# Kernel optimization log

Measured on AMD Instinct MI355X. Metric: run time of the kernel, lower is better.

The kernel has to match this reference:

```python
import jax, jax.numpy as jnp
import numpy as np

H, D_MODEL, D_K, D_V = 16, 1024, 64, 64
B, S = 4, 2048


def _xavier(key, shape):
    # xavier_uniform over last two dims (matches torch for 3D param: fan per matrix)
    fan_in, fan_out = shape[-2], shape[-1]
    limit = jnp.sqrt(6.0 / (fan_in + fan_out))
    return jax.random.uniform(key, shape, jnp.float32, -limit, limit)


def setup_inputs() -> dict:
    key = jax.random.key(0)
    kq, kk, kv, kwq, kwk, kwv, kwo = jax.random.split(key, 7)
    return {
        "Q": jax.random.normal(kq, (B, S, D_MODEL), jnp.float32),
        "K": jax.random.normal(kk, (B, S, D_MODEL), jnp.float32),
        "V": jax.random.normal(kv, (B, S, D_MODEL), jnp.float32),
        "W_Q": _xavier(kwq, (H, D_MODEL, D_K)),
        "W_K": _xavier(kwk, (H, D_MODEL, D_K)),
        "W_V": _xavier(kwv, (H, D_MODEL, D_V)),
        "W_O": _xavier(kwo, (H * D_V, D_MODEL)),
    }


def reference(Q, K, V, W_Q, W_K, W_V, W_O):
    # Per-head projections (batched over heads instead of Python loop)
    q = jnp.einsum("bsm,hmk->bhsk", Q, W_Q)  # [B,H,S,d_k]
    k = jnp.einsum("bsm,hmk->bhsk", K, W_K)  # [B,H,S,d_k]
    v = jnp.einsum("bsm,hmv->bhsv", V, W_V)  # [B,H,S,d_v]

    scale = 1.0 / jnp.sqrt(jnp.asarray(q.shape[-1], q.dtype))
    scores = jnp.einsum("bhqk,bhsk->bhqs", q, k) * scale  # [B,H,S,S]
    attn = jax.nn.softmax(scores, axis=-1)
    heads = jnp.einsum("bhqs,bhsv->bhqv", attn, v)  # [B,H,S,d_v]

    # concat heads along feature dim: [B,S,H*d_v]
    concat = jnp.transpose(heads, (0, 2, 1, 3)).reshape(Q.shape[0], Q.shape[1], -1)
    return concat @ W_O  # [B,S,d_model]
```

## Files before the change

### kernel.cpp

```cpp
#include <hip/hip_runtime.h>
#include <hip/hip_bf16.h>


typedef __attribute__((ext_vector_type(8))) short short8;
typedef __attribute__((ext_vector_type(4))) float floatx4;
typedef unsigned short u16;

#define NH 16
#define DM 1024
#define DK 64
#define NB 4
#define SS 2048

__device__ inline u16 f2bf(float f) {
    unsigned u = __builtin_bit_cast(unsigned, f);
    return (u16)((u + 0x7fffu + ((u >> 16) & 1u)) >> 16);
}

__device__ inline unsigned pk2(float a, float b) {
    unsigned r;
    asm("v_cvt_pk_bf16_f32 %0, %1, %2" : "=v"(r) : "v"(a), "v"(b));
    return r;
}

__device__ inline uint4 cvt8r(float4 lo, float4 hi) {
    uint4 r;
    r.x = pk2(lo.x, lo.y);
    r.y = pk2(lo.z, lo.w);
    r.z = pk2(hi.x, hi.y);
    r.w = pk2(hi.z, hi.w);
    return r;
}

__global__ __launch_bounds__(256) void prep_w(
    const float* __restrict__ W0, const float* __restrict__ W1,
    const float* __restrict__ W2, const float* __restrict__ WO,
    uint4* __restrict__ dst, int mode) {
    int idx = blockIdx.x * 256 + threadIdx.x;
    const int total = mode ? 128 * 1024 : 3 * 16 * 128 * 64;
    const int stride = gridDim.x * 256;
    for (; idx < total; idx += stride) {
        float v[8];
        if (mode == 0) {
            int n64 = idx & 63, kt = (idx >> 6) & 127;
            int h = (idx >> 13) & 15, w = idx >> 17;
            const float* src = (w == 0 ? W0 : (w == 1 ? W1 : W2)) +
                               ((size_t)(h * 1024 + kt * 8)) * 64 + n64;
#pragma unroll
            for (int j = 0; j < 8; j++) v[j] = src[(size_t)j * 64];
        } else {
            int n = idx & 1023, kt = idx >> 10;
            const float* src = WO + (size_t)(kt * 8) * 1024 + n;
#pragma unroll
            for (int j = 0; j < 8; j++) v[j] = src[(size_t)j * 1024];
        }
        uint4 r;
        r.x = pk2(v[0], v[1]);
        r.y = pk2(v[2], v[3]);
        r.z = pk2(v[4], v[5]);
        r.w = pk2(v[6], v[7]);
        dst[idx] = r;
    }
}

__global__ __launch_bounds__(256, 4) void proj_pre(
    const float* __restrict__ X0, const float* __restrict__ X1,
    const float* __restrict__ X2, const uint4* __restrict__ wb,
    u16* __restrict__ outb) {
    __shared__ u16 a_s[64][40];
    const int z = blockIdx.z;
    const float* X = z == 0 ? X0 : (z == 1 ? X1 : X2);
    u16* out = outb + (size_t)z * ((size_t)NB * NH * SS * DK);
    const int mtile = blockIdx.x, ntile = blockIdx.y;
    const int t = threadIdx.x;
    const int w = t >> 6, lane = t & 63, quad = lane >> 4, lr = lane & 15;
    const int ar = t >> 2, ac = (t & 3) * 8;
    const int h = ntile * 2 + (w >> 1);
    const int nh = (w & 1) * 32;
    const size_t bbase = (((size_t)z * 16 + h) * 128 + quad) * 64 + nh + lr;

    float4 axl, axh;
#define PPREFA(kk)                                                             \
    {                                                                          \
        const float* ap = &X[(size_t)(mtile * 64 + ar) * DM + (kk) + ac];      \
        axl = *(const float4*)ap;                                              \
        axh = *(const float4*)(ap + 4);                                        \
    }
    PPREFA(0);
    uint4 bcur[2], bnx[2];
    bcur[0] = wb[bbase];
    bcur[1] = wb[bbase + 16];
    floatx4 acc[4][2] = {};
    for (int kki = 0; kki < DM / 32; kki++) {
        *(uint4*)&a_s[ar][ac] = cvt8r(axl, axh);
        __syncthreads();
        if (kki + 1 < DM / 32) {
            PPREFA((kki + 1) * 32);
            const size_t bi = bbase + (size_t)(kki + 1) * 4 * 64;
            bnx[0] = wb[bi];
            bnx[1] = wb[bi + 16];
        }
        short8 af[4];
#pragma unroll
        for (int i = 0; i < 4; i++)
            af[i] = *(const short8*)&a_s[i * 16 + lr][quad * 8];
#pragma unroll
        for (int i = 0; i < 4; i++)
#pragma unroll
            for (int j = 0; j < 2; j++)
                acc[i][j] = __builtin_amdgcn_mfma_f32_16x16x32_bf16(
                    af[i], __builtin_bit_cast(short8, bcur[j]), acc[i][j],
                    0, 0, 0);
        __syncthreads();
        if (kki + 1 < DM / 32) {
            bcur[0] = bnx[0];
            bcur[1] = bnx[1];
        }
    }
#undef PPREFA

    const int b = (mtile * 64) >> 11;
#pragma unroll
    for (int i = 0; i < 4; i++)
#pragma unroll
        for (int j = 0; j < 2; j++)
#pragma unroll
            for (int rg = 0; rg < 4; rg++) {
                int m = mtile * 64 + i * 16 + quad * 4 + rg;
                int s = m & (SS - 1);
                out[((size_t)(b * NH + h) * SS + s) * DK + nh + j * 16 + lr] =
                    f2bf(acc[i][j][rg]);
            }
}

__global__ __launch_bounds__(256, 4) void oproj_pre(
    const u16* __restrict__ heads,
    const uint4* __restrict__ wob,
    float* __restrict__ out) {
    __shared__ u16 a_s[64][40];
    const int mtile = blockIdx.x, ntile = blockIdx.y;
    const int t = threadIdx.x;
    const int w = t >> 6, lane = t & 63, quad = lane >> 4, lr = lane & 15;
    const int ar = t >> 2, ac = (t & 3) * 8;
    const int b = (mtile * 64) >> 11;
    const int nb = ntile * 128 + w * 32;
    const size_t bbase = (size_t)quad * 1024 + nb + lr;

    uint4 areg;
#define OPREFA(kk)                                                             \
    {                                                                          \
        const int hh = (kk) >> 6, dvb = (kk) & 63;                             \
        int m = mtile * 64 + ar, s = m & (SS - 1);                             \
        areg = *(const uint4*)&heads[((size_t)(b * NH + hh) * SS + s) * DK +   \
                                     dvb + ac];                                \
    }
    OPREFA(0);
    uint4 bcur[2], bnx[2];
    bcur[0] = wob[bbase];
    bcur[1] = wob[bbase + 16];
    floatx4 acc[4][2] = {};
    for (int kki = 0; kki < DM / 32; kki++) {
        *(uint4*)&a_s[ar][ac] = areg;
        __syncthreads();
        if (kki + 1 < DM / 32) {
            OPREFA((kki + 1) * 32);
            const size_t bi = bbase + (size_t)(kki + 1) * 4 * 1024;
            bnx[0] = wob[bi];
            bnx[1] = wob[bi + 16];
        }
        short8 af[4];
#pragma unroll
        for (int i = 0; i < 4; i++)
            af[i] = *(const short8*)&a_s[i * 16 + lr][quad * 8];
#pragma unroll
        for (int i = 0; i < 4; i++)
#pragma unroll
            for (int j = 0; j < 2; j++)
                acc[i][j] = __builtin_amdgcn_mfma_f32_16x16x32_bf16(
                    af[i], __builtin_bit_cast(short8, bcur[j]), acc[i][j],
                    0, 0, 0);
        __syncthreads();
        if (kki + 1 < DM / 32) {
            bcur[0] = bnx[0];
            bcur[1] = bnx[1];
        }
    }
#undef OPREFA

#pragma unroll
    for (int i = 0; i < 4; i++)
#pragma unroll
        for (int j = 0; j < 2; j++)
#pragma unroll
            for (int rg = 0; rg < 4; rg++) {
                int m = mtile * 64 + i * 16 + quad * 4 + rg;
                out[(size_t)m * DM + nb + j * 16 + lr] = acc[i][j][rg];
            }
}

__global__ __launch_bounds__(256, 2) void proj_gemm(
    const float* __restrict__ X,
    const float* __restrict__ W,
    u16* __restrict__ out) {
    __shared__ u16 a_s[128][38];
    __shared__ u16 b_s[128][38];
    const int mtile = blockIdx.x, ntile = blockIdx.y;
    const int t = threadIdx.x;
    const int w = t >> 6, lane = t & 63, quad = lane >> 4, lr = lane & 15;
    const int wm = w & 1, wn = w >> 1;
    const int ar = t >> 2, ac = (t & 3) * 8;
    const int bk = t >> 3, bn = (t & 7) * 8;

    float4 axl[2], axh[2], bwl[2], bwh[2];
#define PROJ_PREF(kk)                                                          \
    {                                                                          \
        _Pragma("unroll") for (int it = 0; it < 2; it++) {                     \
            const float* ap =                                                  \
                &X[(size_t)(mtile * 128 + ar + 64 * it) * DM + (kk) + ac];     \
            axl[it] = *(const float4*)ap;                                      \
            axh[it] = *(const float4*)(ap + 4);                                \
            const float* bp =                                                  \
                &W[((size_t)(ntile * 2 + it) * DM + (kk) + bk) * DK + bn];     \
            bwl[it] = *(const float4*)bp;                                      \
            bwh[it] = *(const float4*)(bp + 4);                                \
        }                                                                      \
    }

    PROJ_PREF(0);
    floatx4 acc[4][4] = {};
    for (int kki = 0; kki < DM / 32; kki++) {
#pragma unroll
        for (int it = 0; it < 2; it++) {
            *(uint4*)&a_s[ar + 64 * it][ac] = cvt8r(axl[it], axh[it]);
            uint4 wv = cvt8r(bwl[it], bwh[it]);
            alignas(16) u16 tmp[8];
            *(uint4*)tmp = wv;
#pragma unroll
            for (int j = 0; j < 8; j++) b_s[64 * it + bn + j][bk] = tmp[j];
        }
        __syncthreads();
        if (kki + 1 < DM / 32) PROJ_PREF((kki + 1) * 32);
        short8 af[4], bf[4];
#pragma unroll
        for (int i = 0; i < 4; i++)
            af[i] = *(const short8*)&a_s[wm * 64 + i * 16 + lr][quad * 8];
#pragma unroll
        for (int j = 0; j < 4; j++)
            bf[j] = *(const short8*)&b_s[wn * 64 + j * 16 + lr][quad * 8];
#pragma unroll
        for (int i = 0; i < 4; i++)
#pragma unroll
            for (int j = 0; j < 4; j++)
                acc[i][j] = __builtin_amdgcn_mfma_f32_16x16x32_bf16(
                    af[i], bf[j], acc[i][j], 0, 0, 0);
        __syncthreads();
    }
#undef PROJ_PREF

    const int b = (mtile * 128) >> 11;
    const int h = ntile * 2 + wn;
#pragma unroll
    for (int i = 0; i < 4; i++)
#pragma unroll
        for (int j = 0; j < 4; j++)
#pragma unroll
            for (int rg = 0; rg < 4; rg++) {
                int m = mtile * 128 + wm * 64 + i * 16 + quad * 4 + rg;
                int s = m & (SS - 1);
                out[((size_t)(b * NH + h) * SS + s) * DK + j * 16 + lr] =
                    f2bf(acc[i][j][rg]);
            }
}

__global__ __launch_bounds__(256) void transpose_v(
    const u16* __restrict__ src, u16* __restrict__ dst) {
    __shared__ u16 ts[64][70];
    const int bh = blockIdx.x, st = blockIdx.y;
    const int t = threadIdx.x;
    const int r = t >> 3, c0 = (t & 7) * 8;
#pragma unroll
    for (int it = 0; it < 2; it++)
        *(uint4*)&ts[r + 32 * it][c0] =
            *(const uint4*)&src[((size_t)bh * SS + st * 64 + r + 32 * it) * DK + c0];
    __syncthreads();
#pragma unroll
    for (int it = 0; it < 2; it++) {
        int dv = r + 32 * it;
        alignas(16) u16 tmp[8];
#pragma unroll
        for (int j = 0; j < 8; j++) tmp[j] = ts[c0 + j][dv];
        *(uint4*)&dst[((size_t)bh * DK + dv) * SS + st * 64 + c0] = *(uint4*)tmp;
    }
}

#define SWZ(r, c) (((r) << 6) + ((c) ^ (((r) & 7) << 3)))

template <bool VT>
__global__ __launch_bounds__(256, 4) void attn_k(
    const u16* q, const u16* __restrict__ k,
    const u16* __restrict__ v, u16* o) {
    __shared__ u16 k_s[64 * 64];
    __shared__ u16 vt_s[64 * 64];

    const int bh = blockIdx.x, qt = blockIdx.y;
    const int t = threadIdx.x;
    const int w = t >> 6, lane = t & 63, quad = lane >> 4, lr = lane & 15;
    const size_t base = (size_t)bh * SS * DK;
    const size_t tbase = (size_t)bh * DK * SS;

    short8 aq[2][2];
#pragma unroll
    for (int qg = 0; qg < 2; qg++) {
        const size_t qrow =
            base + (size_t)(qt * 128 + w * 32 + qg * 16 + lr) * DK;
        aq[qg][0] = *(const short8*)&q[qrow + quad * 8];
        aq[qg][1] = *(const short8*)&q[qrow + 32 + quad * 8];
    }

    floatx4 o_acc[2][4] = {};
    float l0 = 0.f, l1 = 0.f;
    const int sr = t >> 3, sd = (t & 7) * 8;

    const float C1 = 0.18033688f;

    for (int kt = 0; kt < SS / 64; kt++) {
#pragma unroll
        for (int it = 0; it < 2; it++) {
            int r = sr + 32 * it;
            *(uint4*)&k_s[SWZ(r, sd)] =
                *(const uint4*)&k[base + (size_t)(kt * 64 + r) * DK + sd];
            if (VT) {
                *(uint4*)&vt_s[SWZ(r, sd)] =
                    *(const uint4*)&v[tbase + (size_t)r * SS + kt * 64 + sd];
            } else {
                uint4 vv = *(const uint4*)&v[base + (size_t)(kt * 64 + r) * DK + sd];
                alignas(16) u16 tmp[8];
                *(uint4*)tmp = vv;
#pragma unroll
                for (int j = 0; j < 8; j++) vt_s[SWZ(sd + j, r)] = tmp[j];
            }
        }
        __syncthreads();

        floatx4 s0[4] = {}, s1[4] = {};
#pragma unroll
        for (int ks = 0; ks < 2; ks++)
#pragma unroll
            for (int nt = 0; nt < 4; nt++) {
                short8 af =
                    *(const short8*)&k_s[SWZ(nt * 16 + lr, ks * 32 + quad * 8)];
                s0[nt] = __builtin_amdgcn_mfma_f32_16x16x32_bf16(
                    af, aq[0][ks], s0[nt], 0, 0, 0);
                s1[nt] = __builtin_amdgcn_mfma_f32_16x16x32_bf16(
                    af, aq[1][ks], s1[nt], 0, 0, 0);
            }

        unsigned W0[4][2], W1[4][2];
#pragma unroll
        for (int nt = 0; nt < 4; nt++) {
            float p0 = __builtin_amdgcn_exp2f(s0[nt][0] * C1);
            float p1 = __builtin_amdgcn_exp2f(s0[nt][1] * C1);
            float p2 = __builtin_amdgcn_exp2f(s0[nt][2] * C1);
            float p3 = __builtin_amdgcn_exp2f(s0[nt][3] * C1);
            l0 += (p0 + p1) + (p2 + p3);
            W0[nt][0] = pk2(p0, p1);
            W0[nt][1] = pk2(p2, p3);
            float q0 = __builtin_amdgcn_exp2f(s1[nt][0] * C1);
            float q1 = __builtin_amdgcn_exp2f(s1[nt][1] * C1);
            float q2 = __builtin_amdgcn_exp2f(s1[nt][2] * C1);
            float q3 = __builtin_amdgcn_exp2f(s1[nt][3] * C1);
            l1 += (q0 + q1) + (q2 + q3);
            W1[nt][0] = pk2(q0, q1);
            W1[nt][1] = pk2(q2, q3);
        }

        uint4 bf0[2], bf1[2];
#pragma unroll
        for (int ks = 0; ks < 2; ks++) {
            unsigned a0 = W0[2 * ks][0], b0 = W0[2 * ks + 1][0];
            unsigned a1 = W0[2 * ks][1], b1 = W0[2 * ks + 1][1];
            asm("v_permlane32_swap_b32 %0, %1" : "+v"(a0), "+v"(b0));
            asm("v_permlane16_swap_b32 %0, %1" : "+v"(a0), "+v"(b0));
            asm("v_permlane32_swap_b32 %0, %1" : "+v"(a1), "+v"(b1));
            asm("v_permlane16_swap_b32 %0, %1" : "+v"(a1), "+v"(b1));
            bf0[ks].x = a0; bf0[ks].y = a1; bf0[ks].z = b0; bf0[ks].w = b1;
            unsigned c0 = W1[2 * ks][0], d0 = W1[2 * ks + 1][0];
            unsigned c1 = W1[2 * ks][1], d1 = W1[2 * ks + 1][1];
            asm("v_permlane32_swap_b32 %0, %1" : "+v"(c0), "+v"(d0));
            asm("v_permlane16_swap_b32 %0, %1" : "+v"(c0), "+v"(d0));
            asm("v_permlane32_swap_b32 %0, %1" : "+v"(c1), "+v"(d1));
            asm("v_permlane16_swap_b32 %0, %1" : "+v"(c1), "+v"(d1));
            bf1[ks].x = c0; bf1[ks].y = c1; bf1[ks].z = d0; bf1[ks].w = d1;
        }

#pragma unroll
        for (int ks = 0; ks < 2; ks++) {
            short8 p0f = __builtin_bit_cast(short8, bf0[ks]);
            short8 p1f = __builtin_bit_cast(short8, bf1[ks]);
#pragma unroll
            for (int nt = 0; nt < 4; nt++) {
                short8 afv =
                    *(const short8*)&vt_s[SWZ(nt * 16 + lr, ks * 32 + quad * 8)];
                o_acc[0][nt] = __builtin_amdgcn_mfma_f32_16x16x32_bf16(
                    afv, p0f, o_acc[0][nt], 0, 0, 0);
                o_acc[1][nt] = __builtin_amdgcn_mfma_f32_16x16x32_bf16(
                    afv, p1f, o_acc[1][nt], 0, 0, 0);
            }
        }
        __syncthreads();
    }

    l0 += __shfl_xor(l0, 16);
    l0 += __shfl_xor(l0, 32);
    l1 += __shfl_xor(l1, 16);
    l1 += __shfl_xor(l1, 32);
    float inv0 = 1.0f / l0, inv1 = 1.0f / l1;

    const size_t orow0 = base + (size_t)(qt * 128 + w * 32 + lr) * DK;
    const size_t orow1 = orow0 + (size_t)16 * DK;
#pragma unroll
    for (int nt = 0; nt < 4; nt++) {
        uint2 pk;
        pk.x = pk2(o_acc[0][nt][0] * inv0, o_acc[0][nt][1] * inv0);
        pk.y = pk2(o_acc[0][nt][2] * inv0, o_acc[0][nt][3] * inv0);
        *(uint2*)&o[orow0 + nt * 16 + quad * 4] = pk;
        pk.x = pk2(o_acc[1][nt][0] * inv1, o_acc[1][nt][1] * inv1);
        pk.y = pk2(o_acc[1][nt][2] * inv1, o_acc[1][nt][3] * inv1);
        *(uint2*)&o[orow1 + nt * 16 + quad * 4] = pk;
    }
}

__global__ __launch_bounds__(256, 2) void oproj(
    const u16* __restrict__ heads,
    const float* __restrict__ WO,
    float* __restrict__ out) {
    __shared__ u16 a_s[128][38];
    __shared__ u16 b_s[128][38];
    const int mtile = blockIdx.x, ntile = blockIdx.y;
    const int t = threadIdx.x;
    const int w = t >> 6, lane = t & 63, quad = lane >> 4, lr = lane & 15;
    const int wm = w & 1, wn = w >> 1;
    const int ar = t >> 2, ac = (t & 3) * 8;
    const int bk = t >> 3, bn = (t & 7) * 8;
    const int b = (mtile * 128) >> 11;

    uint4 areg[2];
    float4 bwl[2], bwh[2];
#define OP_PREF(kk)                                                            \
    {                                                                          \
        const int h = (kk) >> 6, dvb = (kk) & 63;                              \
        _Pragma("unroll") for (int it = 0; it < 2; it++) {                     \
            int m = mtile * 128 + ar + 64 * it, s = m & (SS - 1);              \
            areg[it] = *(const uint4*)                                         \
                &heads[((size_t)(b * NH + h) * SS + s) * DK + dvb + ac];       \
            const float* bp =                                                  \
                &WO[(size_t)((kk) + bk) * DM + ntile * 128 + 64 * it + bn];    \
            bwl[it] = *(const float4*)bp;                                      \
            bwh[it] = *(const float4*)(bp + 4);                                \
        }                                                                      \
    }

    OP_PREF(0);
    floatx4 acc[4][4] = {};
    for (int kki = 0; kki < DM / 32; kki++) {
#pragma unroll
        for (int it = 0; it < 2; it++) {
            *(uint4*)&a_s[ar + 64 * it][ac] = areg[it];
            uint4 wv = cvt8r(bwl[it], bwh[it]);
            alignas(16) u16 tmp[8];
            *(uint4*)tmp = wv;
#pragma unroll
            for (int j = 0; j < 8; j++) b_s[64 * it + bn + j][bk] = tmp[j];
        }
        __syncthreads();
        if (kki + 1 < DM / 32) OP_PREF((kki + 1) * 32);
        short8 af[4], bf[4];
#pragma unroll
        for (int i = 0; i < 4; i++)
            af[i] = *(const short8*)&a_s[wm * 64 + i * 16 + lr][quad * 8];
#pragma unroll
        for (int j = 0; j < 4; j++)
            bf[j] = *(const short8*)&b_s[wn * 64 + j * 16 + lr][quad * 8];
#pragma unroll
        for (int i = 0; i < 4; i++)
#pragma unroll
            for (int j = 0; j < 4; j++)
                acc[i][j] = __builtin_amdgcn_mfma_f32_16x16x32_bf16(
                    af[i], bf[j], acc[i][j], 0, 0, 0);
        __syncthreads();
    }
#undef OP_PREF

#pragma unroll
    for (int i = 0; i < 4; i++)
#pragma unroll
        for (int j = 0; j < 4; j++)
#pragma unroll
            for (int rg = 0; rg < 4; rg++) {
                int m = mtile * 128 + wm * 64 + i * 16 + quad * 4 + rg;
                int n = ntile * 128 + wn * 64 + j * 16 + lr;
                out[(size_t)m * DM + n] = acc[i][j][rg];
            }
}

extern "C" void kernel_launch(void* const* d_in, const int* in_sizes, int n_in,
                              void* d_out, int out_size, void* d_ws, size_t ws_size,
                              hipStream_t stream) {
    const float* Q  = (const float*)d_in[0];
    const float* K  = (const float*)d_in[1];
    const float* V  = (const float*)d_in[2];
    const float* WQ = (const float*)d_in[3];
    const float* WK = (const float*)d_in[4];
    const float* WV = (const float*)d_in[5];
    const float* WO = (const float*)d_in[6];
    float* out = (float*)d_out;

    char* ws = (char*)d_ws;
    const size_t NQKV = (size_t)NB * NH * SS * DK;
    const size_t SZ = NQKV * 2;
    u16* qp  = (u16*)ws;
    u16* kp  = (u16*)(ws + SZ);
    u16* vp  = (u16*)(ws + 2 * SZ);
    u16* vtp = (u16*)(ws + 3 * SZ);
    u16* hp  = qp;

    const size_t WB_SZ  = 3ull * 16 * 128 * 64 * sizeof(uint4);
    const size_t WOB_SZ = 128ull * 1024 * sizeof(uint4);
    const bool tierA = ws_size >= 4 * SZ + WB_SZ + WOB_SZ;
    const bool tierB = !tierA && ws_size >= 4 * SZ;

    if (tierA || tierB) {
        uint4* wb  = tierA ? (uint4*)(ws + 4 * SZ) : (uint4*)vtp;
        uint4* wob = tierA ? (uint4*)(ws + 4 * SZ + WB_SZ) : (uint4*)kp;

        prep_w<<<1536, 256, 0, stream>>>(WQ, WK, WV, WO, wb, 0);
        if (tierA) prep_w<<<512, 256, 0, stream>>>(WQ, WK, WV, WO, wob, 1);

        proj_pre<<<dim3(NB * SS / 64, DM / 128, 3), 256, 0, stream>>>(
            Q, K, V, wb, qp);
        transpose_v<<<dim3(NB * NH, SS / 64), 256, 0, stream>>>(vp, vtp);
        attn_k<true><<<dim3(NB * NH, SS / 128), 256, 0, stream>>>(
            qp, kp, vtp, hp);
        if (tierB) prep_w<<<512, 256, 0, stream>>>(WQ, WK, WV, WO, wob, 1);
        oproj_pre<<<dim3(NB * SS / 64, DM / 128), 256, 0, stream>>>(
            hp, wob, out);
    } else {
        dim3 pg(NB * SS / 128, DM / 128);
        proj_gemm<<<pg, 256, 0, stream>>>(Q, WQ, qp);
        proj_gemm<<<pg, 256, 0, stream>>>(K, WK, kp);
        proj_gemm<<<pg, 256, 0, stream>>>(V, WV, vp);
        attn_k<false><<<dim3(NB * NH, SS / 128), 256, 0, stream>>>(
            qp, kp, vp, hp);
        oproj<<<dim3(NB * SS / 128, DM / 128), 256, 0, stream>>>(hp, WO, out);
    }
}
```

Baseline: 340.9 us.

## Double-buffer LDS in projection GEMMs, prefetch K/V tiles, and swap grid order

The projection and output-projection GEMMs now use a two-slot LDS A tile with a single custom barrier per k-step instead of two __syncthreads. The grid is reordered so blocks sharing the same activation rows run adjacently, which should improve L2 reuse of X. The attention kernel prefetches the next K/V tile into registers before the QK compute, overlapping global loads with MFMA work. The cost is more register pressure and double the shared memory in the GEMMs.

```diff
diff --git a/kernel.cpp b/kernel.cpp
--- a/kernel.cpp
+++ b/kernel.cpp
@@ -30,6 +30,12 @@
     r.z = pk2(hi.x, hi.y);
     r.w = pk2(hi.z, hi.w);
     return r;
+}
+
+__device__ inline void lds_barrier() {
+    asm volatile("s_waitcnt lgkmcnt(0)" ::: "memory");
+    __builtin_amdgcn_s_barrier();
+    __builtin_amdgcn_sched_barrier(0);
 }
 
 __global__ __launch_bounds__(256) void prep_w(
@@ -67,11 +73,11 @@
     const float* __restrict__ X0, const float* __restrict__ X1,
     const float* __restrict__ X2, const uint4* __restrict__ wb,
     u16* __restrict__ outb) {
-    __shared__ u16 a_s[64][40];
+    __shared__ u16 a_s[2][64][40];
     const int z = blockIdx.z;
     const float* X = z == 0 ? X0 : (z == 1 ? X1 : X2);
     u16* out = outb + (size_t)z * ((size_t)NB * NH * SS * DK);
-    const int mtile = blockIdx.x, ntile = blockIdx.y;
+    const int ntile = blockIdx.x, mtile = blockIdx.y;
     const int t = threadIdx.x;
     const int w = t >> 6, lane = t & 63, quad = lane >> 4, lr = lane & 15;
     const int ar = t >> 2, ac = (t & 3) * 8;
@@ -80,30 +86,32 @@
     const size_t bbase = (((size_t)z * 16 + h) * 128 + quad) * 64 + nh + lr;
 
     float4 axl, axh;
-#define PPREFA(kk)                                                             \
-    {                                                                          \
-        const float* ap = &X[(size_t)(mtile * 64 + ar) * DM + (kk) + ac];      \
-        axl = *(const float4*)ap;                                              \
-        axh = *(const float4*)(ap + 4);                                        \
-    }
-    PPREFA(0);
+    {
+        const float* ap = &X[(size_t)(mtile * 64 + ar) * DM + ac];
+        axl = *(const float4*)ap;
+        axh = *(const float4*)(ap + 4);
+    }
     uint4 bcur[2], bnx[2];
     bcur[0] = wb[bbase];
     bcur[1] = wb[bbase + 16];
     floatx4 acc[4][2] = {};
+    int cur = 0;
     for (int kki = 0; kki < DM / 32; kki++) {
-        *(uint4*)&a_s[ar][ac] = cvt8r(axl, axh);
-        __syncthreads();
+        *(uint4*)&a_s[cur][ar][ac] = cvt8r(axl, axh);
         if (kki + 1 < DM / 32) {
-            PPREFA((kki + 1) * 32);
-            const size_t bi = bbase + (size_t)(kki + 1) * 4 * 64;
+            const float* ap =
+                &X[(size_t)(mtile * 64 + ar) * DM + (kki + 1) * 32 + ac];
+            axl = *(const float4*)ap;
+            axh = *(const float4*)(ap + 4);
+            const size_t bi = bbase + (size_t)(kki + 1) * 256;
             bnx[0] = wb[bi];
             bnx[1] = wb[bi + 16];
         }
+        lds_barrier();
         short8 af[4];
 #pragma unroll
         for (int i = 0; i < 4; i++)
-            af[i] = *(const short8*)&a_s[i * 16 + lr][quad * 8];
+            af[i] = *(const short8*)&a_s[cur][i * 16 + lr][quad * 8];
 #pragma unroll
         for (int i = 0; i < 4; i++)
 #pragma unroll
@@ -111,13 +119,10 @@
                 acc[i][j] = __builtin_amdgcn_mfma_f32_16x16x32_bf16(
                     af[i], __builtin_bit_cast(short8, bcur[j]), acc[i][j],
                     0, 0, 0);
-        __syncthreads();
-        if (kki + 1 < DM / 32) {
-            bcur[0] = bnx[0];
-            bcur[1] = bnx[1];
-        }
-    }
-#undef PPREFA
+        bcur[0] = bnx[0];
+        bcur[1] = bnx[1];
+        cur ^= 1;
+    }
 
     const int b = (mtile * 64) >> 11;
 #pragma unroll
@@ -137,8 +142,8 @@
     const u16* __restrict__ heads,
     const uint4* __restrict__ wob,
     float* __restrict__ out) {
-    __shared__ u16 a_s[64][40];
-    const int mtile = blockIdx.x, ntile = blockIdx.y;
+    __shared__ u16 a_s[2][64][40];
+    const int ntile = blockIdx.x, mtile = blockIdx.y;
     const int t = threadIdx.x;
     const int w = t >> 6, lane = t & 63, quad = lane >> 4, lr = lane & 15;
     const int ar = t >> 2, ac = (t & 3) * 8;
@@ -147,31 +152,32 @@
     const size_t bbase = (size_t)quad * 1024 + nb + lr;
 
     uint4 areg;
-#define OPREFA(kk)                                                             \
-    {                                                                          \
-        const int hh = (kk) >> 6, dvb = (kk) & 63;                             \
-        int m = mtile * 64 + ar, s = m & (SS - 1);                             \
-        areg = *(const uint4*)&heads[((size_t)(b * NH + hh) * SS + s) * DK +   \
-                                     dvb + ac];                                \
-    }
-    OPREFA(0);
+    {
+        int m = mtile * 64 + ar, s = m & (SS - 1);
+        areg = *(const uint4*)&heads[((size_t)(b * NH + 0) * SS + s) * DK + ac];
+    }
     uint4 bcur[2], bnx[2];
     bcur[0] = wob[bbase];
     bcur[1] = wob[bbase + 16];
     floatx4 acc[4][2] = {};
+    int cur = 0;
     for (int kki = 0; kki < DM / 32; kki++) {
-        *(uint4*)&a_s[ar][ac] = areg;
-        __syncthreads();
+        *(uint4*)&a_s[cur][ar][ac] = areg;
         if (kki + 1 < DM / 32) {
-            OPREFA((kki + 1) * 32);
+            const int kk = (kki + 1) * 32;
+            const int hh = kk >> 6, dvb = kk & 63;
+            int m = mtile * 64 + ar, s = m & (SS - 1);
+            areg = *(const uint4*)&heads[((size_t)(b * NH + hh) * SS + s) * DK +
+                                         dvb + ac];
             const size_t bi = bbase + (size_t)(kki + 1) * 4 * 1024;
             bnx[0] = wob[bi];
             bnx[1] = wob[bi + 16];
         }
+        lds_barrier();
         short8 af[4];
 #pragma unroll
         for (int i = 0; i < 4; i++)
-            af[i] = *(const short8*)&a_s[i * 16 + lr][quad * 8];
+            af[i] = *(const short8*)&a_s[cur][i * 16 + lr][quad * 8];
 #pragma unroll
         for (int i = 0; i < 4; i++)
 #pragma unroll
@@ -179,13 +185,10 @@
                 acc[i][j] = __builtin_amdgcn_mfma_f32_16x16x32_bf16(
                     af[i], __builtin_bit_cast(short8, bcur[j]), acc[i][j],
                     0, 0, 0);
-        __syncthreads();
-        if (kki + 1 < DM / 32) {
-            bcur[0] = bnx[0];
-            bcur[1] = bnx[1];
-        }
-    }
-#undef OPREFA
+        bcur[0] = bnx[0];
+        bcur[1] = bnx[1];
+        cur ^= 1;
+    }
 
 #pragma unroll
     for (int i = 0; i < 4; i++)
@@ -323,24 +326,44 @@
 
     const float C1 = 0.18033688f;
 
+    uint4 kr[2], vr[2];
+#pragma unroll
+    for (int it = 0; it < 2; it++) {
+        int r = sr + 32 * it;
+        kr[it] = *(const uint4*)&k[base + (size_t)r * DK + sd];
+        vr[it] = VT ? *(const uint4*)&v[tbase + (size_t)r * SS + sd]
+                    : *(const uint4*)&v[base + (size_t)r * DK + sd];
+    }
+
     for (int kt = 0; kt < SS / 64; kt++) {
 #pragma unroll
         for (int it = 0; it < 2; it++) {
             int r = sr + 32 * it;
-            *(uint4*)&k_s[SWZ(r, sd)] =
-                *(const uint4*)&k[base + (size_t)(kt * 64 + r) * DK + sd];
+            *(uint4*)&k_s[SWZ(r, sd)] = kr[it];
             if (VT) {
-                *(uint4*)&vt_s[SWZ(r, sd)] =
-                    *(const uint4*)&v[tbase + (size_t)r * SS + kt * 64 + sd];
+                *(uint4*)&vt_s[SWZ(r, sd)] = vr[it];
             } else {
-                uint4 vv = *(const uint4*)&v[base + (size_t)(kt * 64 + r) * DK + sd];
                 alignas(16) u16 tmp[8];
-                *(uint4*)tmp = vv;
+                *(uint4*)tmp = vr[it];
 #pragma unroll
                 for (int j = 0; j < 8; j++) vt_s[SWZ(sd + j, r)] = tmp[j];
             }
         }
         __syncthreads();
+
+        if (kt + 1 < SS / 64) {
+#pragma unroll
+            for (int it = 0; it < 2; it++) {
+                int r = sr + 32 * it;
+                kr[it] = *(const uint4*)
+                    &k[base + (size_t)((kt + 1) * 64 + r) * DK + sd];
+                vr[it] = VT
+                    ? *(const uint4*)
+                          &v[tbase + (size_t)r * SS + (kt + 1) * 64 + sd]
+                    : *(const uint4*)
+                          &v[base + (size_t)((kt + 1) * 64 + r) * DK + sd];
+            }
+        }
 
         floatx4 s0[4] = {}, s1[4] = {};
 #pragma unroll
@@ -536,13 +559,13 @@
         prep_w<<<1536, 256, 0, stream>>>(WQ, WK, WV, WO, wb, 0);
         if (tierA) prep_w<<<512, 256, 0, stream>>>(WQ, WK, WV, WO, wob, 1);
 
-        proj_pre<<<dim3(NB * SS / 64, DM / 128, 3), 256, 0, stream>>>(
+        proj_pre<<<dim3(DM / 128, NB * SS / 64, 3), 256, 0, stream>>>(
             Q, K, V, wb, qp);
         transpose_v<<<dim3(NB * NH, SS / 64), 256, 0, stream>>>(vp, vtp);
         attn_k<true><<<dim3(NB * NH, SS / 128), 256, 0, stream>>>(
             qp, kp, vtp, hp);
         if (tierB) prep_w<<<512, 256, 0, stream>>>(WQ, WK, WV, WO, wob, 1);
-        oproj_pre<<<dim3(NB * SS / 64, DM / 128), 256, 0, stream>>>(
+        oproj_pre<<<dim3(DM / 128, NB * SS / 64), 256, 0, stream>>>(
             hp, wob, out);
     } else {
         dim3 pg(NB * SS / 128, DM / 128);
```

New measurement: 428.6 us. 25.7% more time.

## Fold softmax scale into Q projection and process two KV tiles per sync

Applied to the files above, without the earlier changes.

The softmax scale times log2(e) is now applied to Q when the projection output is written, so the attention inner loop calls exp2 directly on the raw scores without a multiply. The attention kernel also loads two 64-key K/V tiles into doubled shared buffers per iteration, which halves the number of barriers and global-load phases. Rounding Q to bf16 after scaling slightly changes numerics. The doubled shared memory (32KB per block) may lower occupancy under the 4-blocks-per-CU launch bound.

```diff
diff --git a/kernel.cpp b/kernel.cpp
--- a/kernel.cpp
+++ b/kernel.cpp
@@ -11,6 +11,8 @@
 #define DK 64
 #define NB 4
 #define SS 2048
+
+#define QSCALE 0.18033688f
 
 __device__ inline u16 f2bf(float f) {
     unsigned u = __builtin_bit_cast(unsigned, f);
@@ -119,6 +121,7 @@
     }
 #undef PPREFA
 
+    const float scl = (z == 0) ? QSCALE : 1.0f;
     const int b = (mtile * 64) >> 11;
 #pragma unroll
     for (int i = 0; i < 4; i++)
@@ -129,7 +132,7 @@
                 int m = mtile * 64 + i * 16 + quad * 4 + rg;
                 int s = m & (SS - 1);
                 out[((size_t)(b * NH + h) * SS + s) * DK + nh + j * 16 + lr] =
-                    f2bf(acc[i][j][rg]);
+                    f2bf(acc[i][j][rg] * scl);
             }
 }
 
@@ -201,7 +204,7 @@
 __global__ __launch_bounds__(256, 2) void proj_gemm(
     const float* __restrict__ X,
     const float* __restrict__ W,
-    u16* __restrict__ out) {
+    u16* __restrict__ out, float scale) {
     __shared__ u16 a_s[128][38];
     __shared__ u16 b_s[128][38];
     const int mtile = blockIdx.x, ntile = blockIdx.y;
@@ -268,7 +271,7 @@
                 int m = mtile * 128 + wm * 64 + i * 16 + quad * 4 + rg;
                 int s = m & (SS - 1);
                 out[((size_t)(b * NH + h) * SS + s) * DK + j * 16 + lr] =
-                    f2bf(acc[i][j][rg]);
+                    f2bf(acc[i][j][rg] * scale);
             }
 }
 
@@ -299,8 +302,8 @@
 __global__ __launch_bounds__(256, 4) void attn_k(
     const u16* q, const u16* __restrict__ k,
     const u16* __restrict__ v, u16* o) {
-    __shared__ u16 k_s[64 * 64];
-    __shared__ u16 vt_s[64 * 64];
+    __shared__ u16 k_s[2][64 * 64];
+    __shared__ u16 vt_s[2][64 * 64];
 
     const int bh = blockIdx.x, qt = blockIdx.y;
     const int t = threadIdx.x;
@@ -321,90 +324,97 @@
     float l0 = 0.f, l1 = 0.f;
     const int sr = t >> 3, sd = (t & 7) * 8;
 
-    const float C1 = 0.18033688f;
-
-    for (int kt = 0; kt < SS / 64; kt++) {
-#pragma unroll
-        for (int it = 0; it < 2; it++) {
-            int r = sr + 32 * it;
-            *(uint4*)&k_s[SWZ(r, sd)] =
-                *(const uint4*)&k[base + (size_t)(kt * 64 + r) * DK + sd];
-            if (VT) {
-                *(uint4*)&vt_s[SWZ(r, sd)] =
-                    *(const uint4*)&v[tbase + (size_t)r * SS + kt * 64 + sd];
-            } else {
-                uint4 vv = *(const uint4*)&v[base + (size_t)(kt * 64 + r) * DK + sd];
-                alignas(16) u16 tmp[8];
-                *(uint4*)tmp = vv;
-#pragma unroll
-                for (int j = 0; j < 8; j++) vt_s[SWZ(sd + j, r)] = tmp[j];
-            }
-        }
-        __syncthreads();
-
-        floatx4 s0[4] = {}, s1[4] = {};
-#pragma unroll
-        for (int ks = 0; ks < 2; ks++)
+    for (int kt = 0; kt < SS / 128; kt++) {
+#pragma unroll
+        for (int u = 0; u < 2; u++) {
+            const int kb = kt * 128 + u * 64;
+#pragma unroll
+            for (int it = 0; it < 2; it++) {
+                int r = sr + 32 * it;
+                *(uint4*)&k_s[u][SWZ(r, sd)] =
+                    *(const uint4*)&k[base + (size_t)(kb + r) * DK + sd];
+                if (VT) {
+                    *(uint4*)&vt_s[u][SWZ(r, sd)] =
+                        *(const uint4*)&v[tbase + (size_t)r * SS + kb + sd];
+                } else {
+                    uint4 vv =
+                        *(const uint4*)&v[base + (size_t)(kb + r) * DK + sd];
+                    alignas(16) u16 tmp[8];
+                    *(uint4*)tmp = vv;
+#pragma unroll
+                    for (int j = 0; j < 8; j++)
+                        vt_s[u][SWZ(sd + j, r)] = tmp[j];
+                }
+            }
+        }
+        __syncthreads();
+
+#pragma unroll
+        for (int u = 0; u < 2; u++) {
+            floatx4 s0[4] = {}, s1[4] = {};
+#pragma unroll
+            for (int ks = 0; ks < 2; ks++)
+#pragma unroll
+                for (int nt = 0; nt < 4; nt++) {
+                    short8 af = *(const short8*)
+                        &k_s[u][SWZ(nt * 16 + lr, ks * 32 + quad * 8)];
+                    s0[nt] = __builtin_amdgcn_mfma_f32_16x16x32_bf16(
+                        af, aq[0][ks], s0[nt], 0, 0, 0);
+                    s1[nt] = __builtin_amdgcn_mfma_f32_16x16x32_bf16(
+                        af, aq[1][ks], s1[nt], 0, 0, 0);
+                }
+
+            unsigned W0[4][2], W1[4][2];
 #pragma unroll
             for (int nt = 0; nt < 4; nt++) {
-                short8 af =
-                    *(const short8*)&k_s[SWZ(nt * 16 + lr, ks * 32 + quad * 8)];
-                s0[nt] = __builtin_amdgcn_mfma_f32_16x16x32_bf16(
-                    af, aq[0][ks], s0[nt], 0, 0, 0);
-                s1[nt] = __builtin_amdgcn_mfma_f32_16x16x32_bf16(
-                    af, aq[1][ks], s1[nt], 0, 0, 0);
-            }
-
-        unsigned W0[4][2], W1[4][2];
-#pragma unroll
-        for (int nt = 0; nt < 4; nt++) {
-            float p0 = __builtin_amdgcn_exp2f(s0[nt][0] * C1);
-            float p1 = __builtin_amdgcn_exp2f(s0[nt][1] * C1);
-            float p2 = __builtin_amdgcn_exp2f(s0[nt][2] * C1);
-            float p3 = __builtin_amdgcn_exp2f(s0[nt][3] * C1);
-            l0 += (p0 + p1) + (p2 + p3);
-            W0[nt][0] = pk2(p0, p1);
-            W0[nt][1] = pk2(p2, p3);
-            float q0 = __builtin_amdgcn_exp2f(s1[nt][0] * C1);
-            float q1 = __builtin_amdgcn_exp2f(s1[nt][1] * C1);
-            float q2 = __builtin_amdgcn_exp2f(s1[nt][2] * C1);
-            float q3 = __builtin_amdgcn_exp2f(s1[nt][3] * C1);
-            l1 += (q0 + q1) + (q2 + q3);
-            W1[nt][0] = pk2(q0, q1);
-            W1[nt][1] = pk2(q2, q3);
-        }
-
-        uint4 bf0[2], bf1[2];
-#pragma unroll
-        for (int ks = 0; ks < 2; ks++) {
-            unsigned a0 = W0[2 * ks][0], b0 = W0[2 * ks + 1][0];
-            unsigned a1 = W0[2 * ks][1], b1 = W0[2 * ks + 1][1];
-            asm("v_permlane32_swap_b32 %0, %1" : "+v"(a0), "+v"(b0));
-            asm("v_permlane16_swap_b32 %0, %1" : "+v"(a0), "+v"(b0));
-            asm("v_permlane32_swap_b32 %0, %1" : "+v"(a1), "+v"(b1));
-            asm("v_permlane16_swap_b32 %0, %1" : "+v"(a1), "+v"(b1));
-            bf0[ks].x = a0; bf0[ks].y = a1; bf0[ks].z = b0; bf0[ks].w = b1;
-            unsigned c0 = W1[2 * ks][0], d0 = W1[2 * ks + 1][0];
-            unsigned c1 = W1[2 * ks][1], d1 = W1[2 * ks + 1][1];
-            asm("v_permlane32_swap_b32 %0, %1" : "+v"(c0), "+v"(d0));
-            asm("v_permlane16_swap_b32 %0, %1" : "+v"(c0), "+v"(d0));
-            asm("v_permlane32_swap_b32 %0, %1" : "+v"(c1), "+v"(d1));
-            asm("v_permlane16_swap_b32 %0, %1" : "+v"(c1), "+v"(d1));
-            bf1[ks].x = c0; bf1[ks].y = c1; bf1[ks].z = d0; bf1[ks].w = d1;
-        }
-
-#pragma unroll
-        for (int ks = 0; ks < 2; ks++) {
-            short8 p0f = __builtin_bit_cast(short8, bf0[ks]);
-            short8 p1f = __builtin_bit_cast(short8, bf1[ks]);
-#pragma unroll
-            for (int nt = 0; nt < 4; nt++) {
-                short8 afv =
-                    *(const short8*)&vt_s[SWZ(nt * 16 + lr, ks * 32 + quad * 8)];
-                o_acc[0][nt] = __builtin_amdgcn_mfma_f32_16x16x32_bf16(
-                    afv, p0f, o_acc[0][nt], 0, 0, 0);
-                o_acc[1][nt] = __builtin_amdgcn_mfma_f32_16x16x32_bf16(
-                    afv, p1f, o_acc[1][nt], 0, 0, 0);
+                float p0 = __builtin_amdgcn_exp2f(s0[nt][0]);
+                float p1 = __builtin_amdgcn_exp2f(s0[nt][1]);
+                float p2 = __builtin_amdgcn_exp2f(s0[nt][2]);
+                float p3 = __builtin_amdgcn_exp2f(s0[nt][3]);
+                l0 += (p0 + p1) + (p2 + p3);
+                W0[nt][0] = pk2(p0, p1);
+                W0[nt][1] = pk2(p2, p3);
+                float q0 = __builtin_amdgcn_exp2f(s1[nt][0]);
+                float q1 = __builtin_amdgcn_exp2f(s1[nt][1]);
+                float q2 = __builtin_amdgcn_exp2f(s1[nt][2]);
+                float q3 = __builtin_amdgcn_exp2f(s1[nt][3]);
+                l1 += (q0 + q1) + (q2 + q3);
+                W1[nt][0] = pk2(q0, q1);
+                W1[nt][1] = pk2(q2, q3);
+            }
+
+            uint4 bf0[2], bf1[2];
+#pragma unroll
+            for (int ks = 0; ks < 2; ks++) {
+                unsigned a0 = W0[2 * ks][0], b0 = W0[2 * ks + 1][0];
+                unsigned a1 = W0[2 * ks][1], b1 = W0[2 * ks + 1][1];
+                asm("v_permlane32_swap_b32 %0, %1" : "+v"(a0), "+v"(b0));
+                asm("v_permlane16_swap_b32 %0, %1" : "+v"(a0), "+v"(b0));
+                asm("v_permlane32_swap_b32 %0, %1" : "+v"(a1), "+v"(b1));
+                asm("v_permlane16_swap_b32 %0, %1" : "+v"(a1), "+v"(b1));
+                bf0[ks].x = a0; bf0[ks].y = a1; bf0[ks].z = b0; bf0[ks].w = b1;
+                unsigned c0 = W1[2 * ks][0], d0 = W1[2 * ks + 1][0];
+                unsigned c1 = W1[2 * ks][1], d1 = W1[2 * ks + 1][1];
+                asm("v_permlane32_swap_b32 %0, %1" : "+v"(c0), "+v"(d0));
+                asm("v_permlane16_swap_b32 %0, %1" : "+v"(c0), "+v"(d0));
+                asm("v_permlane32_swap_b32 %0, %1" : "+v"(c1), "+v"(d1));
+                asm("v_permlane16_swap_b32 %0, %1" : "+v"(c1), "+v"(d1));
+                bf1[ks].x = c0; bf1[ks].y = c1; bf1[ks].z = d0; bf1[ks].w = d1;
+            }
+
+#pragma unroll
+            for (int ks = 0; ks < 2; ks++) {
+                short8 p0f = __builtin_bit_cast(short8, bf0[ks]);
+                short8 p1f = __builtin_bit_cast(short8, bf1[ks]);
+#pragma unroll
+                for (int nt = 0; nt < 4; nt++) {
+                    short8 afv = *(const short8*)
+                        &vt_s[u][SWZ(nt * 16 + lr, ks * 32 + quad * 8)];
+                    o_acc[0][nt] = __builtin_amdgcn_mfma_f32_16x16x32_bf16(
+                        afv, p0f, o_acc[0][nt], 0, 0, 0);
+                    o_acc[1][nt] = __builtin_amdgcn_mfma_f32_16x16x32_bf16(
+                        afv, p1f, o_acc[1][nt], 0, 0, 0);
+                }
             }
         }
         __syncthreads();
@@ -546,9 +556,9 @@
             hp, wob, out);
     } else {
         dim3 pg(NB * SS / 128, DM / 128);
-        proj_gemm<<<pg, 256, 0, stream>>>(Q, WQ, qp);
-        proj_gemm<<<pg, 256, 0, stream>>>(K, WK, kp);
-        proj_gemm<<<pg, 256, 0, stream>>>(V, WV, vp);
+        proj_gemm<<<pg, 256, 0, stream>>>(Q, WQ, qp, QSCALE);
+        proj_gemm<<<pg, 256, 0, stream>>>(K, WK, kp, 1.0f);
+        proj_gemm<<<pg, 256, 0, stream>>>(V, WV, vp, 1.0f);
         attn_k<false><<<dim3(NB * NH, SS / 128), 256, 0, stream>>>(
             qp, kp, vp, hp);
         oproj<<<dim3(NB * SS / 128, DM / 128), 256, 0, stream>>>(hp, WO, out);
```

Result: no change. 345.4 us (+1.3%).
